# Kernel optimization log

Hardware: AMD Instinct MI355X
Metric: run time of the kernel (lower is better)

## Reference

```python
import jax, jax.numpy as jnp
import numpy as np

T, B, NI = 100, 2048, 3
NU = 128          # nh_lstm
NB = 256          # nh_bottleneck
NPC, NHD = 256, 12
INIT = NPC + NHD  # 268


def setup_inputs() -> dict:
    key = jax.random.key(0)
    ks = jax.random.split(key, 20)
    s_in = 1.0 / np.sqrt(NI)
    s_u = 1.0 / np.sqrt(NU)
    s_b = 1.0 / np.sqrt(NB)
    s_e = 1.0 / np.sqrt(INIT)
    return {
        "x": jax.random.normal(ks[0], (T, B, NI), jnp.float32),
        "init_pc": jax.random.normal(ks[1], (B, NPC), jnp.float32),
        "init_hd": jax.random.normal(ks[2], (B, NHD), jnp.float32),
        "Wz": jax.random.normal(ks[3], (NI, NU), jnp.float32) * s_in,
        "Wr": jax.random.normal(ks[4], (NI, NU), jnp.float32) * s_in,
        "Wh": jax.random.normal(ks[5], (NI, NU), jnp.float32) * s_in,
        "Uz": jax.random.normal(ks[6], (NU, NU), jnp.float32) * s_u,
        "Ur": jax.random.normal(ks[7], (NU, NU), jnp.float32) * s_u,
        "Uh": jax.random.normal(ks[8], (NU, NU), jnp.float32) * s_u,
        "bz": jnp.zeros((NU,), jnp.float32),
        "br": jnp.zeros((NU,), jnp.float32),
        "bh": jnp.zeros((NU,), jnp.float32),
        "W_embed": jax.random.normal(ks[9], (INIT, NU), jnp.float32) * s_e,
        "b_embed": jnp.zeros((NU,), jnp.float32),
        "W_bneck": jax.random.normal(ks[10], (NU, NB), jnp.float32) * s_u,  # no bias
        "W_pc": jax.random.normal(ks[11], (NB, NPC), jnp.float32) * s_b,
        "b_pc": jnp.zeros((NPC,), jnp.float32),
        "W_hd": jax.random.normal(ks[12], (NB, NHD), jnp.float32) * s_b,
        "b_hd": jnp.zeros((NHD,), jnp.float32),
    }


def reference(x, init_pc, init_hd, Wz, Wr, Wh, Uz, Ur, Uh, bz, br, bh,
              W_embed, b_embed, W_bneck, W_pc, b_pc, W_hd, b_hd):
    # state_embed(cat(initial_conds))
    init = jnp.concatenate([init_pc, init_hd], axis=1)      # [B, 268]
    h0 = init @ W_embed + b_embed                           # [B, NU]

    # hoist input projections out of the recurrence: [T, B, NU]
    xz = x @ Wz + bz
    xr = x @ Wr + br
    xh = x @ Wh + bh

    def step(h, xs):
        xz_t, xr_t, xh_t = xs
        z = jax.nn.sigmoid(xz_t + h @ Uz)
        r = jax.nn.sigmoid(xr_t + h @ Ur)
        h_tw = jnp.tanh(xh_t + (r * h) @ Uh)
        h = (1.0 - z) * h + z * h_tw
        return h, h

    final_state, states = jax.lax.scan(step, h0, (xz, xr, xh))  # states: [T, B, NU]

    # bottleneck (dropout in eval mode = identity) and logit heads, batched over T
    bottleneck = states @ W_bneck                           # [T, B, NB]
    logits_pc = bottleneck @ W_pc + b_pc                    # [T, B, NPC]
    logits_hd = bottleneck @ W_hd + b_hd                    # [T, B, NHD]
    return logits_hd, logits_pc, bottleneck, states, final_state
```

## Files before the change

### kernel.cpp

```cpp
#include <hip/hip_runtime.h>

#define TT 100
#define BB 2048
#define NI 3
#define NU 128
#define NB 256
#define NPC 256
#define NHD 12

typedef __attribute__((ext_vector_type(8))) short short8;
typedef __attribute__((ext_vector_type(4))) float f32x4;

__device__ __forceinline__ float fast_sigmoid(float x) {
  return 1.0f / (1.0f + __expf(-x));
}
__device__ __forceinline__ float fast_tanh(float x) {
  return 1.0f - 2.0f / (__expf(2.0f * x) + 1.0f);
}
__device__ __forceinline__ short f2bf(float f) {
  uint32_t u = __float_as_uint(f);
  u += 0x7FFF + ((u >> 16) & 1);
  return (short)(u >> 16);
}
__device__ __forceinline__ float bf2f(short s) {
  return __uint_as_float(((uint32_t)(uint16_t)s) << 16);
}

__global__ __launch_bounds__(256) void embed_kernel(
    const float* __restrict__ init_pc, const float* __restrict__ init_hd,
    const float* __restrict__ W_embed, const float* __restrict__ b_embed,
    float* __restrict__ h0) {
  __shared__ float pcs[2][NPC];
  __shared__ float hds[2][NHD];
  const int tid = threadIdx.x;
  const int b0 = blockIdx.x * 2;

  for (int idx = tid; idx < 2 * NPC; idx += 256)
    pcs[idx >> 8][idx & 255] =
        init_pc[(size_t)(b0 + (idx >> 8)) * NPC + (idx & 255)];
  if (tid < 2 * NHD) {
    int rr = tid / NHD, cc = tid - rr * NHD;
    hds[rr][cc] = init_hd[(size_t)(b0 + rr) * NHD + cc];
  }
  __syncthreads();

  const int half = tid >> 7;
  const int j = tid & 127;
  const float* Wp = W_embed + j;
  float a0 = 0.f, a1 = 0.f, a2 = 0.f, a3 = 0.f;
#pragma unroll 4
  for (int k = 0; k < NPC; k += 4) {
    a0 = fmaf(pcs[half][k + 0], Wp[(k + 0) * NU], a0);
    a1 = fmaf(pcs[half][k + 1], Wp[(k + 1) * NU], a1);
    a2 = fmaf(pcs[half][k + 2], Wp[(k + 2) * NU], a2);
    a3 = fmaf(pcs[half][k + 3], Wp[(k + 3) * NU], a3);
  }
#pragma unroll
  for (int k = 0; k < NHD; ++k)
    a0 = fmaf(hds[half][k], Wp[(NPC + k) * NU], a0);
  float acc = b_embed[j] + ((a0 + a1) + (a2 + a3));
  h0[(size_t)(b0 + half) * NU + j] = acc;
}

__global__ __launch_bounds__(512, 2) void gru_mfma_kernel(
    const float* __restrict__ x, const float* __restrict__ h0,
    const float* __restrict__ Wz, const float* __restrict__ Wr,
    const float* __restrict__ Wh, const float* __restrict__ Uz,
    const float* __restrict__ Ur, const float* __restrict__ Uh,
    const float* __restrict__ bz, const float* __restrict__ br,
    const float* __restrict__ bh, float* __restrict__ states,
    float* __restrict__ final_state) {
  __shared__ short h_hi[16 * 128];
  __shared__ short h_lo[16 * 128];
  __shared__ short p_hi[16 * 128];
  __shared__ short p_lo[16 * 128];
  __shared__ float xt_lds[2][8][4];

  const int tid = threadIdx.x;
  const int lane = tid & 63;
  const int w = tid >> 6;
  const int ln15 = lane & 15;
  const int g4 = lane >> 4;
  const int col = w * 16 + ln15;
  const int row0 = blockIdx.x * 8;

  const float wz0 = Wz[col], wz1 = Wz[NU + col], wz2 = Wz[2 * NU + col];
  const float wr0 = Wr[col], wr1 = Wr[NU + col], wr2 = Wr[2 * NU + col];
  const float wh0 = Wh[col], wh1 = Wh[NU + col], wh2 = Wh[2 * NU + col];
  const float bzv = bz[col], brv = br[col], bhv = bh[col];

  short8 Uzh[4], Uzl[4], Urh[4], Url[4], Uhh[4], Uhl[4];
#pragma unroll
  for (int kt = 0; kt < 4; ++kt) {
#pragma unroll
    for (int e = 0; e < 8; ++e) {
      const int kk = kt * 32 + g4 * 8 + e;
      float v;
      short hi;
      v = Uz[kk * NU + col];
      hi = f2bf(v);
      Uzh[kt][e] = hi;
      Uzl[kt][e] = f2bf(v - bf2f(hi));
      v = Ur[kk * NU + col];
      hi = f2bf(v);
      Urh[kt][e] = hi;
      Url[kt][e] = f2bf(v - bf2f(hi));
      v = Uh[kk * NU + col];
      hi = f2bf(v);
      Uhh[kt][e] = hi;
      Uhl[kt][e] = f2bf(v - bf2f(hi));
    }
  }

  float hreg[4];
#pragma unroll
  for (int q = 0; q < 4; ++q) {
    const int row = g4 * 4 + q;
    hreg[q] = (row < 8) ? h0[(size_t)(row0 + row) * NU + col] : 0.0f;
    const int off = row * 256 + ((col * 2) ^ ((row & 7) << 4));
    const short hi = f2bf(hreg[q]);
    *(short*)((char*)h_hi + off) = hi;
    *(short*)((char*)h_lo + off) = f2bf(hreg[q] - bf2f(hi));
  }
  if (tid < 24) {
    const int r = tid / 3, i = tid - r * 3;
    xt_lds[0][r][i] = x[(size_t)(row0 + r) * NI + i];
  }
  __syncthreads();

  for (int t = 0; t < TT; ++t) {
    const int pb = t & 1;

    short8 ahi[4], alo[4];
#pragma unroll
    for (int kt = 0; kt < 4; ++kt) {
      const int off = ln15 * 256 + ((kt * 64 + g4 * 16) ^ ((ln15 & 7) << 4));
      ahi[kt] = *(const short8*)((const char*)h_hi + off);
      alo[kt] = *(const short8*)((const char*)h_lo + off);
    }

    float4 xrow[4];
#pragma unroll
    for (int q = 0; q < 4; ++q)
      xrow[q] = *(const float4*)xt_lds[pb][(g4 * 4 + q) & 7];
    f32x4 zacc, racc;
#pragma unroll
    for (int q = 0; q < 4; ++q) {
      zacc[q] =
          fmaf(xrow[q].x, wz0, fmaf(xrow[q].y, wz1, fmaf(xrow[q].z, wz2, bzv)));
      racc[q] =
          fmaf(xrow[q].x, wr0, fmaf(xrow[q].y, wr1, fmaf(xrow[q].z, wr2, brv)));
    }

#pragma unroll
    for (int kt = 0; kt < 4; ++kt) {
      zacc = __builtin_amdgcn_mfma_f32_16x16x32_bf16(ahi[kt], Uzh[kt], zacc, 0, 0, 0);
      racc = __builtin_amdgcn_mfma_f32_16x16x32_bf16(ahi[kt], Urh[kt], racc, 0, 0, 0);
      zacc = __builtin_amdgcn_mfma_f32_16x16x32_bf16(alo[kt], Uzh[kt], zacc, 0, 0, 0);
      racc = __builtin_amdgcn_mfma_f32_16x16x32_bf16(alo[kt], Urh[kt], racc, 0, 0, 0);
      zacc = __builtin_amdgcn_mfma_f32_16x16x32_bf16(ahi[kt], Uzl[kt], zacc, 0, 0, 0);
      racc = __builtin_amdgcn_mfma_f32_16x16x32_bf16(ahi[kt], Url[kt], racc, 0, 0, 0);
    }

    float zg[4], rh[4];
#pragma unroll
    for (int q = 0; q < 4; ++q) {
      zg[q] = fast_sigmoid(zacc[q]);
      rh[q] = fast_sigmoid(racc[q]) * hreg[q];
    }
    if (g4 < 2) {
#pragma unroll
      for (int q = 0; q < 4; ++q) {
        const int row = g4 * 4 + q;
        const int off = row * 256 + ((col * 2) ^ ((row & 7) << 4));
        const short hi = f2bf(rh[q]);
        *(short*)((char*)p_hi + off) = hi;
        *(short*)((char*)p_lo + off) = f2bf(rh[q] - bf2f(hi));
      }
    }
    __syncthreads();

    if (t + 1 < TT && tid < 24) {
      const int r = tid / 3, i = tid - r * 3;
      xt_lds[pb ^ 1][r][i] = x[(size_t)((t + 1) * BB + row0 + r) * NI + i];
    }

    short8 phi[4], plo[4];
#pragma unroll
    for (int kt = 0; kt < 4; ++kt) {
      const int off = ln15 * 256 + ((kt * 64 + g4 * 16) ^ ((ln15 & 7) << 4));
      phi[kt] = *(const short8*)((const char*)p_hi + off);
      plo[kt] = *(const short8*)((const char*)p_lo + off);
    }
    f32x4 hacc;
#pragma unroll
    for (int q = 0; q < 4; ++q)
      hacc[q] =
          fmaf(xrow[q].x, wh0, fmaf(xrow[q].y, wh1, fmaf(xrow[q].z, wh2, bhv)));
#pragma unroll
    for (int kt = 0; kt < 4; ++kt) {
      hacc = __builtin_amdgcn_mfma_f32_16x16x32_bf16(phi[kt], Uhh[kt], hacc, 0, 0, 0);
      hacc = __builtin_amdgcn_mfma_f32_16x16x32_bf16(plo[kt], Uhh[kt], hacc, 0, 0, 0);
      hacc = __builtin_amdgcn_mfma_f32_16x16x32_bf16(phi[kt], Uhl[kt], hacc, 0, 0, 0);
    }

#pragma unroll
    for (int q = 0; q < 4; ++q) {
      const float htw = fast_tanh(hacc[q]);
      hreg[q] = fmaf(zg[q], htw - hreg[q], hreg[q]);
    }
    if (g4 < 2) {
#pragma unroll
      for (int q = 0; q < 4; ++q) {
        const int row = g4 * 4 + q;
        states[((size_t)t * BB + row0 + row) * NU + col] = hreg[q];
        const int off = row * 256 + ((col * 2) ^ ((row & 7) << 4));
        const short hi = f2bf(hreg[q]);
        *(short*)((char*)h_hi + off) = hi;
        *(short*)((char*)h_lo + off) = f2bf(hreg[q] - bf2f(hi));
      }
    }
    __syncthreads();
  }

  if (g4 < 2) {
#pragma unroll
    for (int q = 0; q < 4; ++q) {
      const int row = g4 * 4 + q;
      final_state[(size_t)(row0 + row) * NU + col] = hreg[q];
    }
  }
}

__global__ __launch_bounds__(256) void prepack_kernel(
    const float* __restrict__ Wb, const float* __restrict__ Wpc,
    const float* __restrict__ Whd, short* __restrict__ Wb_pack,
    short* __restrict__ Wpc_pack, short* __restrict__ Whd_pack) {
  int t = blockIdx.x * 256 + threadIdx.x;
  if (t >= 200 * 64) return;
  int fb = t >> 6, lane = t & 63;
  const float* W;
  short* out;
  int n_tile, k_tile, N, local;
  if (fb < 64) {
    W = Wb; out = Wb_pack; local = fb; n_tile = fb >> 2; k_tile = fb & 3; N = 256;
  } else if (fb < 192) {
    int f = fb - 64;
    W = Wpc; out = Wpc_pack; local = f; n_tile = f >> 3; k_tile = f & 7; N = 256;
  } else {
    int f = fb - 192;
    W = Whd; out = Whd_pack; local = f; n_tile = 0; k_tile = f; N = 12;
  }
  short8 p;
#pragma unroll
  for (int e = 0; e < 8; ++e) {
    int k = k_tile * 32 + (lane >> 4) * 8 + e;
    int colc = n_tile * 16 + (lane & 15);
    float v = (colc < N) ? W[k * N + colc] : 0.0f;
    p[e] = f2bf(v);
  }
  *((short8*)out + (local * 64 + lane)) = p;
}

__global__ __launch_bounds__(256, 3) void heads_mfma_kernel(
    const float* __restrict__ states, const short* __restrict__ Wb_pack,
    const short* __restrict__ Wpc_pack, const short* __restrict__ Whd_pack,
    const float* __restrict__ b_pc, const float* __restrict__ b_hd,
    float* __restrict__ out_hd, float* __restrict__ out_pc,
    float* __restrict__ out_bn) {
  __shared__ short s_lds[64 * 128];
  __shared__ short bn_lds[64 * 256];
  const int tid = threadIdx.x;
  const size_t R0 = (size_t)blockIdx.x * 64;

  for (int c = tid; c < 1024; c += 256) {
    int row = c >> 4, s16 = c & 15;
    const float* src = states + (R0 + row) * 128 + s16 * 8;
    float4 v0 = *(const float4*)src;
    float4 v1 = *(const float4*)(src + 4);
    short8 p;
    p[0] = f2bf(v0.x); p[1] = f2bf(v0.y); p[2] = f2bf(v0.z); p[3] = f2bf(v0.w);
    p[4] = f2bf(v1.x); p[5] = f2bf(v1.y); p[6] = f2bf(v1.z); p[7] = f2bf(v1.w);
    int byte = row * 256 + ((s16 * 16) ^ ((row & 7) << 4));
    *(short8*)((char*)s_lds + byte) = p;
  }
  __syncthreads();

  const int lane = tid & 63;
  const int wave = tid >> 6;
  const int ln15 = lane & 15;
  const int ln4 = lane >> 4;
  const int r0 = wave * 16;

  {
    short8 a[4];
#pragma unroll
    for (int kt = 0; kt < 4; ++kt) {
      int byte =
          (r0 + ln15) * 256 + ((kt * 64 + ln4 * 16) ^ ((ln15 & 7) << 4));
      a[kt] = *(const short8*)((const char*)s_lds + byte);
    }
#pragma unroll
    for (int nt = 0; nt < 16; ++nt) {
      f32x4 acc = {0.f, 0.f, 0.f, 0.f};
      const short8* bp = (const short8*)Wb_pack + (nt * 4) * 64 + lane;
#pragma unroll
      for (int kt = 0; kt < 4; ++kt)
        acc = __builtin_amdgcn_mfma_f32_16x16x32_bf16(a[kt], bp[kt * 64], acc,
                                                      0, 0, 0);
      int colc = nt * 16 + ln15;
#pragma unroll
      for (int q = 0; q < 4; ++q) {
        int row = r0 + ln4 * 4 + q;
        out_bn[(R0 + row) * NB + colc] = acc[q];
        int byte = row * 512 + ((colc * 2) ^ ((row & 7) << 4));
        *(short*)((char*)bn_lds + byte) = f2bf(acc[q]);
      }
    }
  }
  __syncthreads();

  {
    short8 ab[8];
#pragma unroll
    for (int kt = 0; kt < 8; ++kt) {
      int byte =
          (r0 + ln15) * 512 + ((kt * 64 + ln4 * 16) ^ ((ln15 & 7) << 4));
      ab[kt] = *(const short8*)((const char*)bn_lds + byte);
    }
#pragma unroll
    for (int nt = 0; nt < 16; ++nt) {
      int colc = nt * 16 + ln15;
      float bias = b_pc[colc];
      f32x4 acc = {bias, bias, bias, bias};
      const short8* bp = (const short8*)Wpc_pack + (nt * 8) * 64 + lane;
#pragma unroll
      for (int kt = 0; kt < 8; ++kt)
        acc = __builtin_amdgcn_mfma_f32_16x16x32_bf16(ab[kt], bp[kt * 64], acc,
                                                      0, 0, 0);
#pragma unroll
      for (int q = 0; q < 4; ++q)
        out_pc[(R0 + r0 + ln4 * 4 + q) * NPC + colc] = acc[q];
    }
    {
      int colc = ln15;
      float bias = (colc < NHD) ? b_hd[colc] : 0.0f;
      f32x4 acc = {bias, bias, bias, bias};
      const short8* bp = (const short8*)Whd_pack + lane;
#pragma unroll
      for (int kt = 0; kt < 8; ++kt)
        acc = __builtin_amdgcn_mfma_f32_16x16x32_bf16(ab[kt], bp[kt * 64], acc,
                                                      0, 0, 0);
      if (colc < NHD) {
#pragma unroll
        for (int q = 0; q < 4; ++q)
          out_hd[(R0 + r0 + ln4 * 4 + q) * NHD + colc] = acc[q];
      }
    }
  }
}

extern "C" void kernel_launch(void* const* d_in, const int* in_sizes, int n_in,
                              void* d_out, int out_size, void* d_ws,
                              size_t ws_size, hipStream_t stream) {
  (void)in_sizes;
  (void)n_in;
  (void)out_size;
  (void)ws_size;
  const float* x = (const float*)d_in[0];
  const float* init_pc = (const float*)d_in[1];
  const float* init_hd = (const float*)d_in[2];
  const float* Wz = (const float*)d_in[3];
  const float* Wr = (const float*)d_in[4];
  const float* Wh = (const float*)d_in[5];
  const float* Uz = (const float*)d_in[6];
  const float* Ur = (const float*)d_in[7];
  const float* Uh = (const float*)d_in[8];
  const float* bz = (const float*)d_in[9];
  const float* br = (const float*)d_in[10];
  const float* bh = (const float*)d_in[11];
  const float* W_embed = (const float*)d_in[12];
  const float* b_embed = (const float*)d_in[13];
  const float* W_bneck = (const float*)d_in[14];
  const float* W_pc = (const float*)d_in[15];
  const float* b_pc = (const float*)d_in[16];
  const float* W_hd = (const float*)d_in[17];
  const float* b_hd = (const float*)d_in[18];

  float* out = (float*)d_out;
  float* out_hd = out;
  float* out_pc = out_hd + (size_t)TT * BB * NHD;
  float* out_bn = out_pc + (size_t)TT * BB * NPC;
  float* out_st = out_bn + (size_t)TT * BB * NB;
  float* out_fs = out_st + (size_t)TT * BB * NU;

  float* h0 = (float*)d_ws;
  short* Wb_pack = (short*)((char*)d_ws + (1 << 20));
  short* Wpc_pack = Wb_pack + 64 * 64 * 8;
  short* Whd_pack = Wpc_pack + 128 * 64 * 8;

  prepack_kernel<<<50, 256, 0, stream>>>(W_bneck, W_pc, W_hd, Wb_pack,
                                         Wpc_pack, Whd_pack);
  embed_kernel<<<BB / 2, 256, 0, stream>>>(init_pc, init_hd, W_embed, b_embed,
                                           h0);
  gru_mfma_kernel<<<BB / 8, 512, 0, stream>>>(x, h0, Wz, Wr, Wh, Uz, Ur, Uh,
                                              bz, br, bh, out_st, out_fs);
  heads_mfma_kernel<<<(TT * BB) / 64, 256, 0, stream>>>(
      out_st, Wb_pack, Wpc_pack, Whd_pack, b_pc, b_hd, out_hd, out_pc, out_bn);
}
```

Before: 380.5 us.

## Reorder GRU step to shorten serial critical path and preload all inputs to LDS

The recurrent step now computes only the reset gate before the first barrier, moving the update-gate MFMAs after it so they interleave with the candidate MFMAs. Each gate's accumulation is split into two independent MFMA chains to hide MFMA latency. All 100 timesteps of x for the block are preloaded into LDS up front, removing the per-step global load. Barriers become a raw lgkmcnt wait plus s_barrier, so global state stores no longer drain at each barrier; the stores move after the barrier and offsets are hoisted. The cost is more LDS per block and extra accumulator registers.

```diff
diff --git a/kernel.cpp b/kernel.cpp
--- a/kernel.cpp
+++ b/kernel.cpp
@@ -24,6 +24,10 @@
 }
 __device__ __forceinline__ float bf2f(short s) {
   return __uint_as_float(((uint32_t)(uint16_t)s) << 16);
+}
+__device__ __forceinline__ void lds_barrier() {
+  asm volatile("s_waitcnt lgkmcnt(0)" ::: "memory");
+  __builtin_amdgcn_s_barrier();
 }
 
 __global__ __launch_bounds__(256) void embed_kernel(
@@ -74,7 +78,7 @@
   __shared__ short h_lo[16 * 128];
   __shared__ short p_hi[16 * 128];
   __shared__ short p_lo[16 * 128];
-  __shared__ float xt_lds[2][8][4];
+  __shared__ float xs[TT][8][4];
 
   const int tid = threadIdx.x;
   const int lane = tid & 63;
@@ -83,6 +87,11 @@
   const int g4 = lane >> 4;
   const int col = w * 16 + ln15;
   const int row0 = blockIdx.x * 8;
+
+  for (int idx = tid; idx < TT * 32; idx += 512) {
+    const int t = idx >> 5, rem = idx & 31, r = rem >> 2, i = rem & 3;
+    xs[t][r][i] = (i < 3) ? x[(size_t)(t * BB + row0 + r) * NI + i] : 0.0f;
+  }
 
   const float wz0 = Wz[col], wz1 = Wz[NU + col], wz2 = Wz[2 * NU + col];
   const float wr0 = Wr[col], wr1 = Wr[NU + col], wr2 = Wr[2 * NU + col];
@@ -122,113 +131,126 @@
     *(short*)((char*)h_hi + off) = hi;
     *(short*)((char*)h_lo + off) = f2bf(hreg[q] - bf2f(hi));
   }
-  if (tid < 24) {
-    const int r = tid / 3, i = tid - r * 3;
-    xt_lds[0][r][i] = x[(size_t)(row0 + r) * NI + i];
-  }
   __syncthreads();
 
+  int foff[4];
+#pragma unroll
+  for (int kt = 0; kt < 4; ++kt)
+    foff[kt] = ln15 * 256 + ((kt * 64 + g4 * 16) ^ ((ln15 & 7) << 4));
+  int woff[4];
+#pragma unroll
+  for (int q = 0; q < 4; ++q) {
+    const int row = g4 * 4 + q;
+    woff[q] = row * 256 + ((col * 2) ^ ((row & 7) << 4));
+  }
+
   for (int t = 0; t < TT; ++t) {
-    const int pb = t & 1;
-
     short8 ahi[4], alo[4];
 #pragma unroll
     for (int kt = 0; kt < 4; ++kt) {
-      const int off = ln15 * 256 + ((kt * 64 + g4 * 16) ^ ((ln15 & 7) << 4));
-      ahi[kt] = *(const short8*)((const char*)h_hi + off);
-      alo[kt] = *(const short8*)((const char*)h_lo + off);
-    }
-
+      ahi[kt] = *(const short8*)((const char*)h_hi + foff[kt]);
+      alo[kt] = *(const short8*)((const char*)h_lo + foff[kt]);
+    }
     float4 xrow[4];
 #pragma unroll
     for (int q = 0; q < 4; ++q)
-      xrow[q] = *(const float4*)xt_lds[pb][(g4 * 4 + q) & 7];
-    f32x4 zacc, racc;
+      xrow[q] = *(const float4*)xs[t][(g4 * 4 + q) & 7];
+
+    f32x4 r0, r1 = {0.f, 0.f, 0.f, 0.f};
+#pragma unroll
+    for (int q = 0; q < 4; ++q)
+      r0[q] =
+          fmaf(xrow[q].x, wr0, fmaf(xrow[q].y, wr1, fmaf(xrow[q].z, wr2, brv)));
+    r0 = __builtin_amdgcn_mfma_f32_16x16x32_bf16(ahi[0], Urh[0], r0, 0, 0, 0);
+    r1 = __builtin_amdgcn_mfma_f32_16x16x32_bf16(ahi[1], Urh[1], r1, 0, 0, 0);
+    r0 = __builtin_amdgcn_mfma_f32_16x16x32_bf16(alo[0], Urh[0], r0, 0, 0, 0);
+    r1 = __builtin_amdgcn_mfma_f32_16x16x32_bf16(alo[1], Urh[1], r1, 0, 0, 0);
+    r0 = __builtin_amdgcn_mfma_f32_16x16x32_bf16(ahi[0], Url[0], r0, 0, 0, 0);
+    r1 = __builtin_amdgcn_mfma_f32_16x16x32_bf16(ahi[1], Url[1], r1, 0, 0, 0);
+    r0 = __builtin_amdgcn_mfma_f32_16x16x32_bf16(ahi[2], Urh[2], r0, 0, 0, 0);
+    r1 = __builtin_amdgcn_mfma_f32_16x16x32_bf16(ahi[3], Urh[3], r1, 0, 0, 0);
+    r0 = __builtin_amdgcn_mfma_f32_16x16x32_bf16(alo[2], Urh[2], r0, 0, 0, 0);
+    r1 = __builtin_amdgcn_mfma_f32_16x16x32_bf16(alo[3], Urh[3], r1, 0, 0, 0);
+    r0 = __builtin_amdgcn_mfma_f32_16x16x32_bf16(ahi[2], Url[2], r0, 0, 0, 0);
+    r1 = __builtin_amdgcn_mfma_f32_16x16x32_bf16(ahi[3], Url[3], r1, 0, 0, 0);
+
+    if (g4 < 2) {
+#pragma unroll
+      for (int q = 0; q < 4; ++q) {
+        const float rh = fast_sigmoid(r0[q] + r1[q]) * hreg[q];
+        const short hi = f2bf(rh);
+        *(short*)((char*)p_hi + woff[q]) = hi;
+        *(short*)((char*)p_lo + woff[q]) = f2bf(rh - bf2f(hi));
+      }
+    }
+    lds_barrier();
+
+    short8 phi[4], plo[4];
+#pragma unroll
+    for (int kt = 0; kt < 4; ++kt) {
+      phi[kt] = *(const short8*)((const char*)p_hi + foff[kt]);
+      plo[kt] = *(const short8*)((const char*)p_lo + foff[kt]);
+    }
+    f32x4 z0, z1 = {0.f, 0.f, 0.f, 0.f};
+    f32x4 hh0, hh1 = {0.f, 0.f, 0.f, 0.f};
 #pragma unroll
     for (int q = 0; q < 4; ++q) {
-      zacc[q] =
+      z0[q] =
           fmaf(xrow[q].x, wz0, fmaf(xrow[q].y, wz1, fmaf(xrow[q].z, wz2, bzv)));
-      racc[q] =
-          fmaf(xrow[q].x, wr0, fmaf(xrow[q].y, wr1, fmaf(xrow[q].z, wr2, brv)));
-    }
-
-#pragma unroll
-    for (int kt = 0; kt < 4; ++kt) {
-      zacc = __builtin_amdgcn_mfma_f32_16x16x32_bf16(ahi[kt], Uzh[kt], zacc, 0, 0, 0);
-      racc = __builtin_amdgcn_mfma_f32_16x16x32_bf16(ahi[kt], Urh[kt], racc, 0, 0, 0);
-      zacc = __builtin_amdgcn_mfma_f32_16x16x32_bf16(alo[kt], Uzh[kt], zacc, 0, 0, 0);
-      racc = __builtin_amdgcn_mfma_f32_16x16x32_bf16(alo[kt], Urh[kt], racc, 0, 0, 0);
-      zacc = __builtin_amdgcn_mfma_f32_16x16x32_bf16(ahi[kt], Uzl[kt], zacc, 0, 0, 0);
-      racc = __builtin_amdgcn_mfma_f32_16x16x32_bf16(ahi[kt], Url[kt], racc, 0, 0, 0);
-    }
-
-    float zg[4], rh[4];
+      hh0[q] =
+          fmaf(xrow[q].x, wh0, fmaf(xrow[q].y, wh1, fmaf(xrow[q].z, wh2, bhv)));
+    }
+    z0 = __builtin_amdgcn_mfma_f32_16x16x32_bf16(ahi[0], Uzh[0], z0, 0, 0, 0);
+    z1 = __builtin_amdgcn_mfma_f32_16x16x32_bf16(ahi[1], Uzh[1], z1, 0, 0, 0);
+    hh0 = __builtin_amdgcn_mfma_f32_16x16x32_bf16(phi[0], Uhh[0], hh0, 0, 0, 0);
+    hh1 = __builtin_amdgcn_mfma_f32_16x16x32_bf16(phi[1], Uhh[1], hh1, 0, 0, 0);
+    z0 = __builtin_amdgcn_mfma_f32_16x16x32_bf16(alo[0], Uzh[0], z0, 0, 0, 0);
+    z1 = __builtin_amdgcn_mfma_f32_16x16x32_bf16(alo[1], Uzh[1], z1, 0, 0, 0);
+    hh0 = __builtin_amdgcn_mfma_f32_16x16x32_bf16(plo[0], Uhh[0], hh0, 0, 0, 0);
+    hh1 = __builtin_amdgcn_mfma_f32_16x16x32_bf16(plo[1], Uhh[1], hh1, 0, 0, 0);
+    z0 = __builtin_amdgcn_mfma_f32_16x16x32_bf16(ahi[0], Uzl[0], z0, 0, 0, 0);
+    z1 = __builtin_amdgcn_mfma_f32_16x16x32_bf16(ahi[1], Uzl[1], z1, 0, 0, 0);
+    hh0 = __builtin_amdgcn_mfma_f32_16x16x32_bf16(phi[0], Uhl[0], hh0, 0, 0, 0);
+    hh1 = __builtin_amdgcn_mfma_f32_16x16x32_bf16(phi[1], Uhl[1], hh1, 0, 0, 0);
+    z0 = __builtin_amdgcn_mfma_f32_16x16x32_bf16(ahi[2], Uzh[2], z0, 0, 0, 0);
+    z1 = __builtin_amdgcn_mfma_f32_16x16x32_bf16(ahi[3], Uzh[3], z1, 0, 0, 0);
+    hh0 = __builtin_amdgcn_mfma_f32_16x16x32_bf16(phi[2], Uhh[2], hh0, 0, 0, 0);
+    hh1 = __builtin_amdgcn_mfma_f32_16x16x32_bf16(phi[3], Uhh[3], hh1, 0, 0, 0);
+    z0 = __builtin_amdgcn_mfma_f32_16x16x32_bf16(alo[2], Uzh[2], z0, 0, 0, 0);
+    z1 = __builtin_amdgcn_mfma_f32_16x16x32_bf16(alo[3], Uzh[3], z1, 0, 0, 0);
+    hh0 = __builtin_amdgcn_mfma_f32_16x16x32_bf16(plo[2], Uhh[2], hh0, 0, 0, 0);
+    hh1 = __builtin_amdgcn_mfma_f32_16x16x32_bf16(plo[3], Uhh[3], hh1, 0, 0, 0);
+    z0 = __builtin_amdgcn_mfma_f32_16x16x32_bf16(ahi[2], Uzl[2], z0, 0, 0, 0);
+    z1 = __builtin_amdgcn_mfma_f32_16x16x32_bf16(ahi[3], Uzl[3], z1, 0, 0, 0);
+    hh0 = __builtin_amdgcn_mfma_f32_16x16x32_bf16(phi[2], Uhl[2], hh0, 0, 0, 0);
+    hh1 = __builtin_amdgcn_mfma_f32_16x16x32_bf16(phi[3], Uhl[3], hh1, 0, 0, 0);
+
 #pragma unroll
     for (int q = 0; q < 4; ++q) {
-      zg[q] = fast_sigmoid(zacc[q]);
-      rh[q] = fast_sigmoid(racc[q]) * hreg[q];
+      const float zg = fast_sigmoid(z0[q] + z1[q]);
+      const float htw = fast_tanh(hh0[q] + hh1[q]);
+      hreg[q] = fmaf(zg, htw - hreg[q], hreg[q]);
     }
     if (g4 < 2) {
 #pragma unroll
       for (int q = 0; q < 4; ++q) {
-        const int row = g4 * 4 + q;
-        const int off = row * 256 + ((col * 2) ^ ((row & 7) << 4));
-        const short hi = f2bf(rh[q]);
-        *(short*)((char*)p_hi + off) = hi;
-        *(short*)((char*)p_lo + off) = f2bf(rh[q] - bf2f(hi));
+        const short hi = f2bf(hreg[q]);
+        *(short*)((char*)h_hi + woff[q]) = hi;
+        *(short*)((char*)h_lo + woff[q]) = f2bf(hreg[q] - bf2f(hi));
       }
     }
-    __syncthreads();
-
-    if (t + 1 < TT && tid < 24) {
-      const int r = tid / 3, i = tid - r * 3;
-      xt_lds[pb ^ 1][r][i] = x[(size_t)((t + 1) * BB + row0 + r) * NI + i];
-    }
-
-    short8 phi[4], plo[4];
-#pragma unroll
-    for (int kt = 0; kt < 4; ++kt) {
-      const int off = ln15 * 256 + ((kt * 64 + g4 * 16) ^ ((ln15 & 7) << 4));
-      phi[kt] = *(const short8*)((const char*)p_hi + off);
-      plo[kt] = *(const short8*)((const char*)p_lo + off);
-    }
-    f32x4 hacc;
+    lds_barrier();
+    if (g4 < 2) {
+#pragma unroll
+      for (int q = 0; q < 4; ++q)
+        states[((size_t)t * BB + row0 + g4 * 4 + q) * NU + col] = hreg[q];
+    }
+  }
+
+  if (g4 < 2) {
 #pragma unroll
     for (int q = 0; q < 4; ++q)
-      hacc[q] =
-          fmaf(xrow[q].x, wh0, fmaf(xrow[q].y, wh1, fmaf(xrow[q].z, wh2, bhv)));
-#pragma unroll
-    for (int kt = 0; kt < 4; ++kt) {
-      hacc = __builtin_amdgcn_mfma_f32_16x16x32_bf16(phi[kt], Uhh[kt], hacc, 0, 0, 0);
-      hacc = __builtin_amdgcn_mfma_f32_16x16x32_bf16(plo[kt], Uhh[kt], hacc, 0, 0, 0);
-      hacc = __builtin_amdgcn_mfma_f32_16x16x32_bf16(phi[kt], Uhl[kt], hacc, 0, 0, 0);
-    }
-
-#pragma unroll
-    for (int q = 0; q < 4; ++q) {
-      const float htw = fast_tanh(hacc[q]);
-      hreg[q] = fmaf(zg[q], htw - hreg[q], hreg[q]);
-    }
-    if (g4 < 2) {
-#pragma unroll
-      for (int q = 0; q < 4; ++q) {
-        const int row = g4 * 4 + q;
-        states[((size_t)t * BB + row0 + row) * NU + col] = hreg[q];
-        const int off = row * 256 + ((col * 2) ^ ((row & 7) << 4));
-        const short hi = f2bf(hreg[q]);
-        *(short*)((char*)h_hi + off) = hi;
-        *(short*)((char*)h_lo + off) = f2bf(hreg[q] - bf2f(hi));
-      }
-    }
-    __syncthreads();
-  }
-
-  if (g4 < 2) {
-#pragma unroll
-    for (int q = 0; q < 4; ++q) {
-      const int row = g4 * 4 + q;
-      final_state[(size_t)(row0 + row) * NU + col] = hreg[q];
-    }
+      final_state[(size_t)(row0 + g4 * 4 + q) * NU + col] = hreg[q];
   }
 }
 
```

New measurement: 382.1 us. About the same (+0.4%).
